# Performance work log

Hardware: AMD Instinct MI355X
Metric: run time of the kernel (lower is better)

Reference implementation:

```python
import jax, jax.numpy as jnp
import numpy as np

B, H, S, D = 2, 16, 2048, 128


def setup_inputs() -> dict:
    key = jax.random.key(0)
    kq, kk, kv = jax.random.split(key, 3)
    q = jax.random.normal(kq, (B, H, S, D), dtype=jnp.float32)
    k = jax.random.normal(kk, (B, H, S, D), dtype=jnp.float32)
    v = jax.random.normal(kv, (B, H, S, D), dtype=jnp.float32)
    scale = jnp.float32(1.0 / np.sqrt(D))
    return {"q": q, "k": k, "v": v, "scale": scale}


def reference(q, k, v, scale):
    # scores: [B, H, S, S]
    attn = jnp.einsum("bhqd,bhkd->bhqk", q, k) * scale
    attn = jnp.square(jax.nn.relu(attn))  # relu(x)^2 score function (no softmax)
    return jnp.einsum("bhqk,bhkd->bhqd", attn, v)
```

## Files before the change

### kernel.cpp

```cpp
#include <hip/hip_runtime.h>
#include <hip/hip_bf16.h>
#include <stdint.h>

#define S_LEN 2048
#define D_DIM 128
#define QT 128
#define KT 64
#define NT (S_LEN/KT)
#define TKT 32
#define TNT (S_LEN/TKT)

typedef float  f32x4  __attribute__((ext_vector_type(4)));
typedef float  f32x16 __attribute__((ext_vector_type(16)));
typedef short  bf16x8 __attribute__((ext_vector_type(8)));
typedef unsigned int uintx4 __attribute__((ext_vector_type(4)));

__device__ __forceinline__ short f2bf(float f) {
    return __builtin_bit_cast(short, __float2bfloat16(f));
}

__device__ __forceinline__ unsigned int pk2(float lo, float hi) {
    unsigned int d;
    asm("v_cvt_pk_bf16_f32 %0, %1, %2" : "=v"(d) : "v"(lo), "v"(hi));
    return d;
}

__device__ __forceinline__ void gload_lds16(const short* g, char* l) {
    __builtin_amdgcn_global_load_lds(
        (const __attribute__((address_space(1))) void*)g,
        (__attribute__((address_space(3))) void*)l,
        16, 0, 0);
}

__global__ __launch_bounds__(256)
void convert_k_kernel(const float* __restrict__ kin, short* __restrict__ kbf) {
    const size_t i = ((size_t)blockIdx.x * 256 + threadIdx.x) * 8;
    f32x4 a = *(const f32x4*)(kin + i);
    f32x4 c = *(const f32x4*)(kin + i + 4);
    bf16x8 t;
    t[0]=f2bf(a[0]); t[1]=f2bf(a[1]); t[2]=f2bf(a[2]); t[3]=f2bf(a[3]);
    t[4]=f2bf(c[0]); t[5]=f2bf(c[1]); t[6]=f2bf(c[2]); t[7]=f2bf(c[3]);
    *(bf16x8*)(kbf + i) = t;
}

__global__ __launch_bounds__(256)
void transpose_v_kernel(const float* __restrict__ vin, short* __restrict__ vt) {
    __shared__ short T[16 * 130];
    const int tid = threadIdx.x;
    const int blk = blockIdx.x;
    const int bh  = blk >> 3;
    const int d0  = (blk & 7) * 16;
    const float* vb = vin + (size_t)bh * S_LEN * D_DIM;
    short* vtb = vt + (size_t)bh * (size_t)D_DIM * S_LEN;
    const int c4 = tid & 3;
    const int rr = tid >> 2;
    const int dl = tid >> 4;
    const int kc = tid & 15;

    for (int kc0 = 0; kc0 < S_LEN; kc0 += 128) {
        #pragma unroll
        for (int h = 0; h < 2; ++h) {
            const int krow = kc0 + h*64 + rr;
            f32x4 a = *(const f32x4*)(vb + (size_t)krow * D_DIM + d0 + c4*4);
            #pragma unroll
            for (int j = 0; j < 4; ++j)
                T[(c4*4 + j)*130 + h*64 + rr] = f2bf(a[j]);
        }
        __syncthreads();
        int w0 = *(const int*)&T[dl*130 + kc*8 + 0];
        int w1 = *(const int*)&T[dl*130 + kc*8 + 2];
        int w2 = *(const int*)&T[dl*130 + kc*8 + 4];
        int w3 = *(const int*)&T[dl*130 + kc*8 + 6];
        int4 val = make_int4(w0, w1, w2, w3);
        *(int4*)(vtb + (size_t)(d0 + dl) * S_LEN + kc0 + kc*8) = val;
        __syncthreads();
    }
}

__global__ __launch_bounds__(256, 3)
void relu2_attn_main(const float* __restrict__ q,
                     const short* __restrict__ kbf,
                     const short* __restrict__ vtbf,
                     const float* __restrict__ scale_p,
                     float* __restrict__ out) {
    __shared__ __align__(16) char lds[49152];

    const int tid  = threadIdx.x;
    const int wave = tid >> 6;
    const int lane = tid & 63;
    const int l31  = lane & 31;
    const int hi   = lane >> 5;

    const int bid = blockIdx.x;
    const int bh  = bid & 31;
    const int qt  = bid >> 5;
    const int q0  = qt * QT;

    const float* qb = q    + (size_t)bh * S_LEN * D_DIM;
    const short* kb = kbf  + (size_t)bh * S_LEN * D_DIM;
    const short* vt = vtbf + (size_t)bh * (size_t)D_DIM * S_LEN;
    float*       ob = out  + (size_t)bh * S_LEN * D_DIM;

    const float scale = scale_p[0];

    const int RB = hi*512 + l31*16;

    int kOff[2], vOff[2];
    #pragma unroll
    for (int p = 0; p < 2; ++p) {
        const int s = (p*4 + wave)*64 + lane;
        kOff[p] = (s & 31)*128 + (s >> 6)*16 + ((s >> 5) & 1)*8;
        vOff[p] = ((s >> 7)*32 + (s & 31))*2048
                + ((s >> 6) & 1)*16 + ((s >> 5) & 1)*8;
    }

    bf16x8 qa[8];
    {
        const int qrow = q0 + wave*32 + l31;
        const float* qp = qb + (size_t)qrow * D_DIM + hi*8;
        #pragma unroll
        for (int dk = 0; dk < 8; ++dk) {
            f32x4 a = *(const f32x4*)(qp + dk*16);
            f32x4 c = *(const f32x4*)(qp + dk*16 + 4);
            bf16x8 t;
            t[0]=f2bf(a[0]*scale); t[1]=f2bf(a[1]*scale);
            t[2]=f2bf(a[2]*scale); t[3]=f2bf(a[3]*scale);
            t[4]=f2bf(c[0]*scale); t[5]=f2bf(c[1]*scale);
            t[6]=f2bf(c[2]*scale); t[7]=f2bf(c[3]*scale);
            qa[dk] = t;
        }
    }

    f32x16 oacc[4];
    #pragma unroll
    for (int df = 0; df < 4; ++df) oacc[df] = {};

#define STAGE(T, CB) do {                                                     \
    const int k0_ = (T) * TKT;                                                \
    _Pragma("unroll")                                                         \
    for (int p_ = 0; p_ < 2; ++p_) {                                          \
        const int ch_ = p_*4 + wave;                                          \
        gload_lds16(kb + (size_t)k0_*128 + kOff[p_],                          \
                    lds + (CB) + ch_*1024);                                   \
        gload_lds16(vt + k0_ + vOff[p_],                                      \
                    lds + (CB) + 8192 + ch_*1024);                            \
    }                                                                         \
} while (0)

#define TILE_COMPUTE(CB) do {                                                 \
    f32x16 s0 = {};                                                           \
    __builtin_amdgcn_s_setprio(1);                                            \
    _Pragma("unroll")                                                         \
    for (int dk = 0; dk < 8; ++dk) {                                          \
        bf16x8 a = *(const bf16x8*)(lds + (CB) + RB + (dk<<10));              \
        s0 = __builtin_amdgcn_mfma_f32_32x32x16_bf16(a, qa[dk], s0, 0, 0, 0); \
    }                                                                         \
    __builtin_amdgcn_s_setprio(0);                                            \
    bf16x8 pa[2];                                                             \
    {                                                                         \
        float pr[16];                                                         \
        _Pragma("unroll")                                                     \
        for (int r = 0; r < 16; ++r) {                                        \
            float m_ = fmaxf(s0[r], 0.f); pr[r] = m_ * m_;                    \
        }                                                                     \
        _Pragma("unroll")                                                     \
        for (int t2 = 0; t2 < 2; ++t2) {                                      \
            unsigned int X  = pk2(pr[8*t2+0], pr[8*t2+1]);                    \
            unsigned int Y  = pk2(pr[8*t2+4], pr[8*t2+5]);                    \
            unsigned int X2 = pk2(pr[8*t2+2], pr[8*t2+3]);                    \
            unsigned int Y2 = pk2(pr[8*t2+6], pr[8*t2+7]);                    \
            asm volatile("v_permlane32_swap_b32 %0, %1" : "+v"(X),  "+v"(Y)); \
            asm volatile("v_permlane32_swap_b32 %0, %1" : "+v"(X2), "+v"(Y2));\
            pa[t2] = __builtin_bit_cast(bf16x8, (uintx4){X, X2, Y, Y2});      \
        }                                                                     \
    }                                                                         \
    __builtin_amdgcn_s_setprio(1);                                            \
    _Pragma("unroll")                                                         \
    for (int s_ = 0; s_ < 2; ++s_) {                                          \
        _Pragma("unroll")                                                     \
        for (int df = 0; df < 4; ++df) {                                      \
            bf16x8 vf = *(const bf16x8*)(lds + (CB) + 8192 + RB               \
                                         + (df<<11) + (s_<<10));              \
            oacc[df] = __builtin_amdgcn_mfma_f32_32x32x16_bf16(               \
                           pa[s_], vf, oacc[df], 0, 0, 0);                    \
        }                                                                     \
    }                                                                         \
    __builtin_amdgcn_s_setprio(0);                                            \
} while (0)

    STAGE(0, 0);
    STAGE(1, 16384);

    int c0 = 0, c1 = 16384, c2 = 32768;

    #pragma unroll 1
    for (int t = 0; t < TNT; ++t) {
        asm volatile("s_waitcnt vmcnt(4)" ::: "memory");
        __builtin_amdgcn_s_barrier();
        __builtin_amdgcn_sched_barrier(0);
        STAGE((t + 2) & (TNT - 1), c2);
        TILE_COMPUTE(c0);
        const int tmp = c0; c0 = c1; c1 = c2; c2 = tmp;
    }

    asm volatile("s_waitcnt vmcnt(0)" ::: "memory");

    #pragma unroll
    for (int df = 0; df < 4; ++df) {
        #pragma unroll
        for (int rg = 0; rg < 4; ++rg) {
            #pragma unroll
            for (int e = 0; e < 4; ++e) {
                const int row = q0 + wave*32 + rg*8 + hi*4 + e;
                ob[(size_t)row * D_DIM + df*32 + l31] = oacc[df][rg*4 + e];
            }
        }
    }
}

#define KS 136
#define VS 72
#define PS 72

__global__ __launch_bounds__(256, 2)
void relu2_attn_fallback(const float* __restrict__ q,
                         const float* __restrict__ k,
                         const float* __restrict__ v,
                         const float* __restrict__ scale_p,
                         float* __restrict__ out) {
    __shared__ short Klds[KT][KS];
    __shared__ short VTlds[D_DIM][VS];
    __shared__ short Plds[QT][PS];

    const int tid  = threadIdx.x;
    const int wave = tid >> 6;
    const int lane = tid & 63;
    const int l15  = lane & 15;
    const int lg   = lane >> 4;

    const int bid = blockIdx.x;
    const int bh  = bid & 31;
    const int qt  = bid >> 5;
    const int q0  = qt * QT;

    const float* qb = q + (size_t)bh * S_LEN * D_DIM;
    const float* kb = k + (size_t)bh * S_LEN * D_DIM;
    const float* vb = v + (size_t)bh * S_LEN * D_DIM;
    float*       ob = out + (size_t)bh * S_LEN * D_DIM;

    const float scale = scale_p[0];

    bf16x8 qa[2][4];
    {
        const int qrow = q0 + wave * 32;
        #pragma unroll
        for (int qf = 0; qf < 2; ++qf) {
            const float* qp = qb + (size_t)(qrow + qf*16 + l15) * D_DIM + lg * 8;
            #pragma unroll
            for (int dk = 0; dk < 4; ++dk) {
                f32x4 a = *(const f32x4*)(qp + dk*32);
                f32x4 c = *(const f32x4*)(qp + dk*32 + 4);
                bf16x8 t;
                t[0]=f2bf(a[0]*scale); t[1]=f2bf(a[1]*scale);
                t[2]=f2bf(a[2]*scale); t[3]=f2bf(a[3]*scale);
                t[4]=f2bf(c[0]*scale); t[5]=f2bf(c[1]*scale);
                t[6]=f2bf(c[2]*scale); t[7]=f2bf(c[3]*scale);
                qa[qf][dk] = t;
            }
        }
    }

    const int kr = tid >> 4;
    const int kc = tid & 15;
    const int vd = tid & 127;
    const int vh = (tid >> 7) * 32;

    f32x4 kreg[8];
    float vreg[32];

#define FLOAD_TILE(T) do {                                                    \
    const float* kp_ = kb + (size_t)((T) * KT) * D_DIM;                       \
    _Pragma("unroll")                                                         \
    for (int p = 0; p < 4; ++p) {                                             \
        const float* rp_ = kp_ + (size_t)(p*16 + kr) * D_DIM + kc*8;          \
        kreg[2*p]   = *(const f32x4*)rp_;                                     \
        kreg[2*p+1] = *(const f32x4*)(rp_ + 4);                               \
    }                                                                         \
    const float* vp_ = vb + (size_t)((T) * KT + vh) * D_DIM + vd;             \
    _Pragma("unroll")                                                         \
    for (int j = 0; j < 32; ++j) vreg[j] = vp_[(size_t)j * D_DIM];            \
} while (0)

#define FSTORE_TILE() do {                                                    \
    _Pragma("unroll")                                                         \
    for (int p = 0; p < 4; ++p) {                                             \
        f32x4 a_ = kreg[2*p], b_ = kreg[2*p+1];                               \
        bf16x8 w_;                                                            \
        w_[0]=f2bf(a_[0]); w_[1]=f2bf(a_[1]); w_[2]=f2bf(a_[2]); w_[3]=f2bf(a_[3]); \
        w_[4]=f2bf(b_[0]); w_[5]=f2bf(b_[1]); w_[6]=f2bf(b_[2]); w_[7]=f2bf(b_[3]); \
        *(bf16x8*)&Klds[p*16 + kr][kc*8] = w_;                                \
    }                                                                         \
    _Pragma("unroll")                                                         \
    for (int c = 0; c < 4; ++c) {                                             \
        bf16x8 w_;                                                            \
        w_[0]=f2bf(vreg[c*8+0]); w_[1]=f2bf(vreg[c*8+1]);                     \
        w_[2]=f2bf(vreg[c*8+2]); w_[3]=f2bf(vreg[c*8+3]);                     \
        w_[4]=f2bf(vreg[c*8+4]); w_[5]=f2bf(vreg[c*8+5]);                     \
        w_[6]=f2bf(vreg[c*8+6]); w_[7]=f2bf(vreg[c*8+7]);                     \
        *(bf16x8*)&VTlds[vd][vh + c*8] = w_;                                  \
    }                                                                         \
} while (0)

    f32x4 oacc[2][8];
    #pragma unroll
    for (int i = 0; i < 2; ++i)
        #pragma unroll
        for (int j = 0; j < 8; ++j)
            oacc[i][j] = f32x4{0.f, 0.f, 0.f, 0.f};

    FLOAD_TILE(0);

    for (int t = 0; t < NT; ++t) {
        FSTORE_TILE();
        __syncthreads();
        FLOAD_TILE((t + 1) & (NT - 1));

        f32x4 sacc[2][4];
        #pragma unroll
        for (int qf = 0; qf < 2; ++qf)
            #pragma unroll
            for (int kf = 0; kf < 4; ++kf)
                sacc[qf][kf] = f32x4{0.f, 0.f, 0.f, 0.f};

        #pragma unroll
        for (int dk = 0; dk < 4; ++dk) {
            #pragma unroll
            for (int kf = 0; kf < 4; ++kf) {
                bf16x8 bf = *(const bf16x8*)&Klds[kf*16 + l15][dk*32 + lg*8];
                #pragma unroll
                for (int qf = 0; qf < 2; ++qf)
                    sacc[qf][kf] = __builtin_amdgcn_mfma_f32_16x16x32_bf16(
                        qa[qf][dk], bf, sacc[qf][kf], 0, 0, 0);
            }
        }

        #pragma unroll
        for (int qf = 0; qf < 2; ++qf) {
            #pragma unroll
            for (int kf = 0; kf < 4; ++kf) {
                f32x4 sv = sacc[qf][kf];
                #pragma unroll
                for (int e = 0; e < 4; ++e) {
                    float r = fmaxf(sv[e], 0.f);
                    Plds[wave*32 + qf*16 + lg*4 + e][kf*16 + l15] = f2bf(r * r);
                }
            }
        }

        #pragma unroll
        for (int ks = 0; ks < 2; ++ks) {
            bf16x8 pa[2];
            #pragma unroll
            for (int qf = 0; qf < 2; ++qf)
                pa[qf] = *(const bf16x8*)&Plds[wave*32 + qf*16 + l15][ks*32 + lg*8];
            #pragma unroll
            for (int df = 0; df < 8; ++df) {
                bf16x8 vf = *(const bf16x8*)&VTlds[df*16 + l15][ks*32 + lg*8];
                #pragma unroll
                for (int qf = 0; qf < 2; ++qf)
                    oacc[qf][df] = __builtin_amdgcn_mfma_f32_16x16x32_bf16(
                        pa[qf], vf, oacc[qf][df], 0, 0, 0);
            }
        }
        __syncthreads();
    }

    #pragma unroll
    for (int qf = 0; qf < 2; ++qf) {
        #pragma unroll
        for (int df = 0; df < 8; ++df) {
            f32x4 o = oacc[qf][df];
            const int row = q0 + wave*32 + qf*16 + lg*4;
            float* op = ob + (size_t)row * D_DIM + df*16 + l15;
            op[0*D_DIM] = o[0];
            op[1*D_DIM] = o[1];
            op[2*D_DIM] = o[2];
            op[3*D_DIM] = o[3];
        }
    }
}

extern "C" void kernel_launch(void* const* d_in, const int* in_sizes, int n_in,
                              void* d_out, int out_size, void* d_ws, size_t ws_size,
                              hipStream_t stream) {
    const float* q = (const float*)d_in[0];
    const float* k = (const float*)d_in[1];
    const float* v = (const float*)d_in[2];
    const float* scale = (const float*)d_in[3];
    float* out = (float*)d_out;

    const size_t elems = (size_t)2 * 16 * S_LEN * D_DIM;
    const size_t need  = elems * 2 * 2;

    if (ws_size >= need) {
        short* kbf = (short*)d_ws;
        short* vtb = (short*)d_ws + elems;
        convert_k_kernel<<<dim3((int)(elems / (256 * 8))), dim3(256), 0, stream>>>(k, kbf);
        transpose_v_kernel<<<dim3(256), dim3(256), 0, stream>>>(v, vtb);
        relu2_attn_main<<<dim3(512), dim3(256), 0, stream>>>(q, kbf, vtb, scale, out);
    } else {
        relu2_attn_fallback<<<dim3(512), dim3(256), 0, stream>>>(q, k, v, scale, out);
    }
}
```

Measured before the change: 101.7 us.

## Split key range across two wave groups per block with LDS reduction

```diff
diff --git a/kernel.cpp b/kernel.cpp
--- a/kernel.cpp
+++ b/kernel.cpp
@@ -23,6 +23,11 @@
     unsigned int d;
     asm("v_cvt_pk_bf16_f32 %0, %1, %2" : "=v"(d) : "v"(lo), "v"(hi));
     return d;
+}
+
+__device__ __forceinline__ float r2(float x) {
+    float m = fmaxf(x, 0.f);
+    return m * m;
 }
 
 __device__ __forceinline__ void gload_lds16(const short* g, char* l) {
@@ -77,19 +82,21 @@
     }
 }
 
-__global__ __launch_bounds__(256, 3)
+__global__ __launch_bounds__(512, 4)
 void relu2_attn_main(const float* __restrict__ q,
                      const short* __restrict__ kbf,
                      const short* __restrict__ vtbf,
                      const float* __restrict__ scale_p,
                      float* __restrict__ out) {
-    __shared__ __align__(16) char lds[49152];
+    __shared__ __align__(16) char lds[65536];
 
     const int tid  = threadIdx.x;
     const int wave = tid >> 6;
     const int lane = tid & 63;
     const int l31  = lane & 31;
     const int hi   = lane >> 5;
+    const int w4   = wave & 3;
+    const int grp  = wave >> 2;
 
     const int bid = blockIdx.x;
     const int bh  = bid & 31;
@@ -104,11 +111,13 @@
     const float scale = scale_p[0];
 
     const int RB = hi*512 + l31*16;
+    const int GB = grp * 32768;
+    const int tb = grp * 32;
 
     int kOff[2], vOff[2];
     #pragma unroll
     for (int p = 0; p < 2; ++p) {
-        const int s = (p*4 + wave)*64 + lane;
+        const int s = (p*4 + w4)*64 + lane;
         kOff[p] = (s & 31)*128 + (s >> 6)*16 + ((s >> 5) & 1)*8;
         vOff[p] = ((s >> 7)*32 + (s & 31))*2048
                 + ((s >> 6) & 1)*16 + ((s >> 5) & 1)*8;
@@ -116,7 +125,7 @@
 
     bf16x8 qa[8];
     {
-        const int qrow = q0 + wave*32 + l31;
+        const int qrow = q0 + w4*32 + l31;
         const float* qp = qb + (size_t)qrow * D_DIM + hi*8;
         #pragma unroll
         for (int dk = 0; dk < 8; ++dk) {
@@ -135,11 +144,11 @@
     #pragma unroll
     for (int df = 0; df < 4; ++df) oacc[df] = {};
 
-#define STAGE(T, CB) do {                                                     \
-    const int k0_ = (T) * TKT;                                                \
+#define STAGE(TI, CB) do {                                                    \
+    const int k0_ = (TI) * TKT;                                               \
     _Pragma("unroll")                                                         \
     for (int p_ = 0; p_ < 2; ++p_) {                                          \
-        const int ch_ = p_*4 + wave;                                          \
+        const int ch_ = p_*4 + w4;                                            \
         gload_lds16(kb + (size_t)k0_*128 + kOff[p_],                          \
                     lds + (CB) + ch_*1024);                                   \
         gload_lds16(vt + k0_ + vOff[p_],                                      \
@@ -157,22 +166,15 @@
     }                                                                         \
     __builtin_amdgcn_s_setprio(0);                                            \
     bf16x8 pa[2];                                                             \
-    {                                                                         \
-        float pr[16];                                                         \
-        _Pragma("unroll")                                                     \
-        for (int r = 0; r < 16; ++r) {                                        \
-            float m_ = fmaxf(s0[r], 0.f); pr[r] = m_ * m_;                    \
-        }                                                                     \
-        _Pragma("unroll")                                                     \
-        for (int t2 = 0; t2 < 2; ++t2) {                                      \
-            unsigned int X  = pk2(pr[8*t2+0], pr[8*t2+1]);                    \
-            unsigned int Y  = pk2(pr[8*t2+4], pr[8*t2+5]);                    \
-            unsigned int X2 = pk2(pr[8*t2+2], pr[8*t2+3]);                    \
-            unsigned int Y2 = pk2(pr[8*t2+6], pr[8*t2+7]);                    \
-            asm volatile("v_permlane32_swap_b32 %0, %1" : "+v"(X),  "+v"(Y)); \
-            asm volatile("v_permlane32_swap_b32 %0, %1" : "+v"(X2), "+v"(Y2));\
-            pa[t2] = __builtin_bit_cast(bf16x8, (uintx4){X, X2, Y, Y2});      \
-        }                                                                     \
+    _Pragma("unroll")                                                         \
+    for (int t2 = 0; t2 < 2; ++t2) {                                          \
+        unsigned int X  = pk2(r2(s0[8*t2+0]), r2(s0[8*t2+1]));                \
+        unsigned int Y  = pk2(r2(s0[8*t2+4]), r2(s0[8*t2+5]));                \
+        unsigned int X2 = pk2(r2(s0[8*t2+2]), r2(s0[8*t2+3]));                \
+        unsigned int Y2 = pk2(r2(s0[8*t2+6]), r2(s0[8*t2+7]));                \
+        asm volatile("v_permlane32_swap_b32 %0, %1" : "+v"(X),  "+v"(Y));     \
+        asm volatile("v_permlane32_swap_b32 %0, %1" : "+v"(X2), "+v"(Y2));    \
+        pa[t2] = __builtin_bit_cast(bf16x8, (uintx4){X, X2, Y, Y2});          \
     }                                                                         \
     __builtin_amdgcn_s_setprio(1);                                            \
     _Pragma("unroll")                                                         \
@@ -188,33 +190,44 @@
     __builtin_amdgcn_s_setprio(0);                                            \
 } while (0)
 
-    STAGE(0, 0);
-    STAGE(1, 16384);
-
-    int c0 = 0, c1 = 16384, c2 = 32768;
+    STAGE(tb, GB);
 
     #pragma unroll 1
-    for (int t = 0; t < TNT; ++t) {
-        asm volatile("s_waitcnt vmcnt(4)" ::: "memory");
-        __builtin_amdgcn_s_barrier();
-        __builtin_amdgcn_sched_barrier(0);
-        STAGE((t + 2) & (TNT - 1), c2);
-        TILE_COMPUTE(c0);
-        const int tmp = c0; c0 = c1; c1 = c2; c2 = tmp;
-    }
-
-    asm volatile("s_waitcnt vmcnt(0)" ::: "memory");
-
-    #pragma unroll
-    for (int df = 0; df < 4; ++df) {
-        #pragma unroll
-        for (int rg = 0; rg < 4; ++rg) {
-            #pragma unroll
-            for (int e = 0; e < 4; ++e) {
-                const int row = q0 + wave*32 + rg*8 + hi*4 + e;
-                ob[(size_t)row * D_DIM + df*32 + l31] = oacc[df][rg*4 + e];
-            }
-        }
+    for (int p = 0; p < 16; ++p) {
+        __syncthreads();
+        STAGE(tb + 2*p + 1, GB + 16384);
+        TILE_COMPUTE(GB);
+        __syncthreads();
+        STAGE(tb + ((2*p + 2) & 31), GB);
+        TILE_COMPUTE(GB + 16384);
+    }
+
+    __syncthreads();
+    float* Fl = (float*)lds;
+    if (grp == 1) {
+        #pragma unroll
+        for (int df = 0; df < 4; ++df)
+            #pragma unroll
+            for (int rg = 0; rg < 4; ++rg)
+                #pragma unroll
+                for (int e = 0; e < 4; ++e)
+                    Fl[w4*4096 + (rg*8 + hi*4 + e)*128 + df*32 + l31]
+                        = oacc[df][rg*4 + e];
+    }
+    __syncthreads();
+    if (grp == 0) {
+        #pragma unroll
+        for (int df = 0; df < 4; ++df)
+            #pragma unroll
+            for (int rg = 0; rg < 4; ++rg)
+                #pragma unroll
+                for (int e = 0; e < 4; ++e) {
+                    const int qr = rg*8 + hi*4 + e;
+                    const int row = q0 + w4*32 + qr;
+                    ob[(size_t)row * D_DIM + df*32 + l31]
+                        = oacc[df][rg*4 + e]
+                        + Fl[w4*4096 + qr*128 + df*32 + l31];
+                }
     }
 }
 
@@ -407,7 +420,7 @@
         short* vtb = (short*)d_ws + elems;
         convert_k_kernel<<<dim3((int)(elems / (256 * 8))), dim3(256), 0, stream>>>(k, kbf);
         transpose_v_kernel<<<dim3(256), dim3(256), 0, stream>>>(v, vtb);
-        relu2_attn_main<<<dim3(512), dim3(256), 0, stream>>>(q, kbf, vtb, scale, out);
+        relu2_attn_main<<<dim3(512), dim3(512), 0, stream>>>(q, kbf, vtb, scale, out);
     } else {
         relu2_attn_fallback<<<dim3(512), dim3(256), 0, stream>>>(q, k, v, scale, out);
     }
```

New measurement: 127.6 us. 1.25x slower.
